# Kernel tuning notes

Hardware: AMD Instinct MI355X
Metric: run time of the kernel (lower is better)

The kernel has to match this reference:

```python
import jax, jax.numpy as jnp
import numpy as np

D_MODEL = 1024
NHEAD = 16
HEAD_DIM = D_MODEL // NHEAD


def setup_inputs() -> dict:
    key = jax.random.key(0)
    ks = jax.random.split(key, 9)
    s = 0.02
    x = jax.random.normal(ks[0], (2, 2048, D_MODEL), dtype=jnp.float32)
    Wq = jax.random.normal(ks[1], (D_MODEL, D_MODEL), dtype=jnp.float32) * s
    bq = jnp.zeros((D_MODEL,), jnp.float32)
    Wk = jax.random.normal(ks[2], (D_MODEL, D_MODEL), dtype=jnp.float32) * s
    bk = jnp.zeros((D_MODEL,), jnp.float32)
    Wv = jax.random.normal(ks[3], (D_MODEL, D_MODEL), dtype=jnp.float32) * s
    bv = jnp.zeros((D_MODEL,), jnp.float32)
    Wo = jax.random.normal(ks[4], (D_MODEL, D_MODEL), dtype=jnp.float32) * s
    bo = jnp.zeros((D_MODEL,), jnp.float32)
    return {"x": x, "Wq": Wq, "bq": bq, "Wk": Wk, "bk": bk,
            "Wv": Wv, "bv": bv, "Wo": Wo, "bo": bo}


def _rope(x, sin, cos):
    # x: [B, L, H, Dh]; rotate-half as in the torch module
    half = x.shape[-1] // 2
    x1, x2 = x[..., :half], x[..., half:]
    rotated = jnp.concatenate([-x2, x1], axis=-1)
    return x * cos + rotated * sin


def reference(x, Wq, bq, Wk, bk, Wv, bv, Wo, bo):
    B, L, D = x.shape
    H, Dh = NHEAD, HEAD_DIM
    q = (x @ Wq.T + bq).reshape(B, L, H, Dh)
    k = (x @ Wk.T + bk).reshape(B, L, H, Dh)
    v = (x @ Wv.T + bv).reshape(B, L, H, Dh)

    inv_freq = 1.0 / (10000.0 ** (jnp.arange(0, Dh, 2, dtype=jnp.float32) / Dh))
    t = jnp.arange(L, dtype=jnp.float32)
    freqs = jnp.einsum('i,j->ij', t, inv_freq)          # [L, Dh/2]
    emb = jnp.concatenate([freqs, freqs], axis=-1)      # [L, Dh]
    cos = jnp.cos(emb)[None, :, None, :]
    sin = jnp.sin(emb)[None, :, None, :]

    q = _rope(q, sin, cos)
    k = _rope(k, sin, cos)

    # [B, H, L, L]
    scores = jnp.einsum('bqhd,bkhd->bhqk', q, k) / jnp.sqrt(jnp.float32(Dh))
    attn = jax.nn.softmax(scores, axis=-1)
    # dropout in eval mode = identity (p given as 0.0)
    out = jnp.einsum('bhqk,bkhd->bqhd', attn, v).reshape(B, L, D)
    return out @ Wo.T + bo
```

## Files before the change

### kernel.cpp

```cpp
#include <hip/hip_runtime.h>
#include <math.h>

#define D_MODEL 1024
#define NHEAD 16
#define HEAD_DIM 64
#define L_SEQ 2048
#define BATCH 2
#define M_ROWS 4096
#define SC_Q 0.18033688011112042f

typedef __attribute__((ext_vector_type(8))) short short8;
typedef __attribute__((ext_vector_type(4))) float floatx4;

__device__ inline unsigned f2bf_u(float x) {
    unsigned u = __float_as_uint(x);
    return (u + 0x7fffu + ((u >> 16) & 1u)) >> 16;
}

__device__ inline void gl_lds16(const void* g, void* l) {
    __builtin_amdgcn_global_load_lds((const __attribute__((address_space(1))) void*)g,
                                     (__attribute__((address_space(3))) void*)l, 16, 0, 0);
}

__global__ __launch_bounds__(256) void cvt_all(
    const float* __restrict__ x,  const float* __restrict__ wq,
    const float* __restrict__ wk, const float* __restrict__ wv,
    const float* __restrict__ wo,
    unsigned short* __restrict__ xb,  unsigned short* __restrict__ wqb,
    unsigned short* __restrict__ wkb, unsigned short* __restrict__ wvb,
    unsigned short* __restrict__ wob, float* __restrict__ rt) {
    if (blockIdx.y == 5) {
        for (int idx = blockIdx.x * 256 + threadIdx.x; idx < L_SEQ * 16;
             idx += gridDim.x * 256) {
            int l = idx >> 4, f = idx & 15;
            float if0 = (float)pow(10000.0, -(double)f / 32.0);
            float if1 = (float)pow(10000.0, -(double)(f + 16) / 32.0);
            float s0, c0, s1, c1;
            sincosf((float)l * if0, &s0, &c0);
            sincosf((float)l * if1, &s1, &c1);
            float4 v = {c0, c1, s0, s1};
            *(float4*)(rt + (size_t)idx * 4) = v;
        }
        return;
    }
    const float* s; unsigned short* d; int n;
    switch (blockIdx.y) {
        case 0:  s = x;  d = xb;  n = M_ROWS * D_MODEL; break;
        case 1:  s = wq; d = wqb; n = D_MODEL * D_MODEL; break;
        case 2:  s = wk; d = wkb; n = D_MODEL * D_MODEL; break;
        case 3:  s = wv; d = wvb; n = D_MODEL * D_MODEL; break;
        default: s = wo; d = wob; n = D_MODEL * D_MODEL; break;
    }
    int stride = gridDim.x * 256 * 4;
    for (int i = (blockIdx.x * 256 + threadIdx.x) * 4; i < n; i += stride) {
        float4 v = *(const float4*)(s + i);
        ushort4 o;
        o.x = (unsigned short)f2bf_u(v.x);
        o.y = (unsigned short)f2bf_u(v.y);
        o.z = (unsigned short)f2bf_u(v.z);
        o.w = (unsigned short)f2bf_u(v.w);
        *(ushort4*)(d + i) = o;
    }
}

__global__ __launch_bounds__(256) void gemm_qkv(
    const unsigned short* __restrict__ xb,
    const unsigned short* __restrict__ wqb, const unsigned short* __restrict__ wkb,
    const unsigned short* __restrict__ wvb,
    const float* __restrict__ bq, const float* __restrict__ bk,
    const float* __restrict__ bv, const float* __restrict__ rt,
    unsigned short* __restrict__ qo, unsigned short* __restrict__ ko,
    unsigned short* __restrict__ vo) {
    __shared__ __align__(16) unsigned short As[128 * 32];
    __shared__ __align__(16) unsigned short Bs[128 * 32];

    const int K = D_MODEL;
    const int tid = threadIdx.x;
    const int lane = tid & 63;
    const int w = tid >> 6;
    const int wm = (w & 1) * 64;
    const int wn = (w >> 1) * 64;
    const int m0 = blockIdx.x * 128;
    const int n0 = blockIdx.y * 128;

    const unsigned short* Wsel; const float* bsel;
    unsigned short* osel; int mode; float oscale;
    if (blockIdx.z == 0)      { Wsel = wqb; bsel = bq; osel = qo; mode = 1; oscale = SC_Q; }
    else if (blockIdx.z == 1) { Wsel = wkb; bsel = bk; osel = ko; mode = 1; oscale = 1.0f; }
    else                      { Wsel = wvb; bsel = bv; osel = vo; mode = 2; oscale = 1.0f; }

    floatx4 acc[4][4];
#pragma unroll
    for (int i = 0; i < 4; ++i)
#pragma unroll
        for (int j = 0; j < 4; ++j) acc[i][j] = (floatx4){0.f, 0.f, 0.f, 0.f};

    const int sr = lane >> 2;
    const int ss = lane & 3;
    const unsigned short* Ag = xb + (size_t)m0 * K;
    const unsigned short* Bg = Wsel + (size_t)n0 * K;

    for (int k0 = 0; k0 < K; k0 += 32) {
        __syncthreads();
#pragma unroll
        for (int t = 0; t < 2; ++t) {
            int R0 = t * 64 + w * 16;
            int r = R0 + sr;
            int c = ss ^ ((r >> 1) & 3);
            gl_lds16(Ag + (size_t)r * K + k0 + c * 8, (void*)(As + R0 * 32));
            gl_lds16(Bg + (size_t)r * K + k0 + c * 8, (void*)(Bs + R0 * 32));
        }
        __syncthreads();

        short8 af[4], bf[4];
#pragma unroll
        for (int mt = 0; mt < 4; ++mt) {
            int ar = wm + mt * 16 + (lane & 15);
            int slot = (lane >> 4) ^ ((ar >> 1) & 3);
            af[mt] = *(const short8*)(As + ar * 32 + slot * 8);
        }
#pragma unroll
        for (int nt = 0; nt < 4; ++nt) {
            int br = wn + nt * 16 + (lane & 15);
            int slot = (lane >> 4) ^ ((br >> 1) & 3);
            bf[nt] = *(const short8*)(Bs + br * 32 + slot * 8);
        }
#pragma unroll
        for (int mt = 0; mt < 4; ++mt)
#pragma unroll
            for (int nt = 0; nt < 4; ++nt)
                acc[mt][nt] = __builtin_amdgcn_mfma_f32_16x16x32_bf16(
                    af[mt], bf[nt], acc[mt][nt], 0, 0, 0);
    }

#pragma unroll
    for (int nt = 0; nt < 4; ++nt) {
        float bn = bsel[n0 + wn + nt * 16 + (lane & 15)];
#pragma unroll
        for (int mt = 0; mt < 4; ++mt)
#pragma unroll
            for (int i = 0; i < 4; ++i) acc[mt][nt][i] += bn;
    }

    const int h = (n0 + wn) >> 6;

    if (mode == 1) {
#pragma unroll
        for (int mt = 0; mt < 4; ++mt)
#pragma unroll
            for (int i = 0; i < 4; ++i) {
                int m = m0 + wm + mt * 16 + (lane >> 4) * 4 + i;
                int b = m >> 11, l = m & (L_SEQ - 1);
                float4 tc = *(const float4*)(rt + ((size_t)(l * 16 + (lane & 15)) << 2));
#pragma unroll
                for (int nt = 0; nt < 4; ++nt) {
                    int dh = nt * 16 + (lane & 15);
                    float partner = acc[mt][nt ^ 2][i];
                    float rot = (nt < 2) ? -partner : partner;
                    float c = (nt & 1) ? tc.y : tc.x;
                    float s = (nt & 1) ? tc.w : tc.z;
                    float val = (acc[mt][nt][i] * c + rot * s) * oscale;
                    size_t idx = (((size_t)(b * NHEAD + h)) * L_SEQ + l) * HEAD_DIM + dh;
                    osel[idx] = (unsigned short)f2bf_u(val);
                }
            }
    } else {
#pragma unroll
        for (int mt = 0; mt < 4; ++mt)
#pragma unroll
            for (int ih = 0; ih < 4; ih += 2) {
                int m = m0 + wm + mt * 16 + (lane >> 4) * 4 + ih;
                int b = m >> 11, l = m & (L_SEQ - 1);
#pragma unroll
                for (int nt = 0; nt < 4; ++nt) {
                    int dh = nt * 16 + (lane & 15);
                    unsigned v0 = f2bf_u(acc[mt][nt][ih]);
                    unsigned v1 = f2bf_u(acc[mt][nt][ih + 1]);
                    size_t idx = (((size_t)(b * NHEAD + h)) * HEAD_DIM + dh) * L_SEQ + l;
                    *(unsigned*)(vo + idx) = v0 | (v1 << 16);
                }
            }
    }
}

__global__ __launch_bounds__(256) void gemm_out(
    const unsigned short* __restrict__ A, const unsigned short* __restrict__ Wb,
    const float* __restrict__ bias, float* __restrict__ out) {
    __shared__ __align__(16) unsigned short As[128 * 32];
    __shared__ __align__(16) unsigned short Bs[128 * 32];

    const int K = D_MODEL;
    const int tid = threadIdx.x;
    const int lane = tid & 63;
    const int w = tid >> 6;
    const int wm = (w & 1) * 64;
    const int wn = (w >> 1) * 64;
    const int m0 = blockIdx.x * 128;
    const int n0 = blockIdx.y * 128;

    floatx4 acc[4][4];
#pragma unroll
    for (int i = 0; i < 4; ++i)
#pragma unroll
        for (int j = 0; j < 4; ++j) acc[i][j] = (floatx4){0.f, 0.f, 0.f, 0.f};

    const int sr = lane >> 2;
    const int ss = lane & 3;
    const unsigned short* Ag = A + (size_t)m0 * K;
    const unsigned short* Bg = Wb + (size_t)n0 * K;

    for (int k0 = 0; k0 < K; k0 += 32) {
        __syncthreads();
#pragma unroll
        for (int t = 0; t < 2; ++t) {
            int R0 = t * 64 + w * 16;
            int r = R0 + sr;
            int c = ss ^ ((r >> 1) & 3);
            gl_lds16(Ag + (size_t)r * K + k0 + c * 8, (void*)(As + R0 * 32));
            gl_lds16(Bg + (size_t)r * K + k0 + c * 8, (void*)(Bs + R0 * 32));
        }
        __syncthreads();

        short8 af[4], bf[4];
#pragma unroll
        for (int mt = 0; mt < 4; ++mt) {
            int ar = wm + mt * 16 + (lane & 15);
            int slot = (lane >> 4) ^ ((ar >> 1) & 3);
            af[mt] = *(const short8*)(As + ar * 32 + slot * 8);
        }
#pragma unroll
        for (int nt = 0; nt < 4; ++nt) {
            int br = wn + nt * 16 + (lane & 15);
            int slot = (lane >> 4) ^ ((br >> 1) & 3);
            bf[nt] = *(const short8*)(Bs + br * 32 + slot * 8);
        }
#pragma unroll
        for (int mt = 0; mt < 4; ++mt)
#pragma unroll
            for (int nt = 0; nt < 4; ++nt)
                acc[mt][nt] = __builtin_amdgcn_mfma_f32_16x16x32_bf16(
                    af[mt], bf[nt], acc[mt][nt], 0, 0, 0);
    }

#pragma unroll
    for (int nt = 0; nt < 4; ++nt) {
        int n = n0 + wn + nt * 16 + (lane & 15);
        float bn = bias[n];
#pragma unroll
        for (int mt = 0; mt < 4; ++mt)
#pragma unroll
            for (int i = 0; i < 4; ++i) {
                int m = m0 + wm + mt * 16 + (lane >> 4) * 4 + i;
                out[(size_t)m * D_MODEL + n] = acc[mt][nt][i] + bn;
            }
    }
}

__global__ __launch_bounds__(256) void attn_mfma(
    const unsigned short* __restrict__ q, const unsigned short* __restrict__ k,
    const unsigned short* __restrict__ vt, unsigned short* __restrict__ out) {
    __shared__ __align__(16) unsigned short Ks[2][64 * 64];
    __shared__ __align__(16) unsigned short Vs[2][64 * 64];
    __shared__ __align__(16) unsigned short Ps[4 * 32 * 72];

    const int tid = threadIdx.x;
    const int lane = tid & 63;
    const int w = tid >> 6;
    const int bh = blockIdx.y;
    const int q0 = blockIdx.x * 128;

    const unsigned short* qb = q + (size_t)bh * L_SEQ * HEAD_DIM;
    const unsigned short* kb = k + (size_t)bh * L_SEQ * HEAD_DIM;
    const unsigned short* vb = vt + (size_t)bh * HEAD_DIM * L_SEQ;

    short8 qf[2][2];
#pragma unroll
    for (int mt = 0; mt < 2; ++mt)
#pragma unroll
        for (int ks = 0; ks < 2; ++ks)
            qf[mt][ks] = *(const short8*)(
                qb + (size_t)(q0 + w * 32 + mt * 16 + (lane & 15)) * HEAD_DIM
                + ks * 32 + (lane >> 4) * 8);

    floatx4 o[2][4];
    float lsum[2][4];
#pragma unroll
    for (int mt = 0; mt < 2; ++mt)
#pragma unroll
        for (int j = 0; j < 4; ++j) {
            o[mt][j] = (floatx4){0.f, 0.f, 0.f, 0.f};
            lsum[mt][j & 3] = 0.f;
        }

    unsigned short* Psw = Ps + w * (32 * 72);
    const int sr = lane >> 3;
    const int ss = lane & 7;
    const int T = L_SEQ / 64;

#pragma unroll
    for (int t = 0; t < 2; ++t) {
        int R0 = t * 32 + w * 8;
        int r = R0 + sr;
        int c = ss ^ (r & 7);
        gl_lds16(kb + (size_t)r * HEAD_DIM + c * 8, (void*)(Ks[0] + R0 * 64));
        gl_lds16(vb + (size_t)r * L_SEQ + c * 8, (void*)(Vs[0] + R0 * 64));
    }

    for (int t = 0; t < T; ++t) {
        __syncthreads();
        if (t + 1 < T) {
            int kv1 = (t + 1) * 64;
            int nb = (t + 1) & 1;
#pragma unroll
            for (int tt = 0; tt < 2; ++tt) {
                int R0 = tt * 32 + w * 8;
                int r = R0 + sr;
                int c = ss ^ (r & 7);
                gl_lds16(kb + (size_t)(kv1 + r) * HEAD_DIM + c * 8, (void*)(Ks[nb] + R0 * 64));
                gl_lds16(vb + (size_t)r * L_SEQ + kv1 + c * 8, (void*)(Vs[nb] + R0 * 64));
            }
        }
        const unsigned short* Kc = Ks[t & 1];
        const unsigned short* Vc = Vs[t & 1];

        floatx4 s[2][4];
#pragma unroll
        for (int mt = 0; mt < 2; ++mt)
#pragma unroll
            for (int nt = 0; nt < 4; ++nt) s[mt][nt] = (floatx4){0.f, 0.f, 0.f, 0.f};
#pragma unroll
        for (int ks = 0; ks < 2; ++ks)
#pragma unroll
            for (int nt = 0; nt < 4; ++nt) {
                int br = nt * 16 + (lane & 15);
                int slot = (ks * 4 + (lane >> 4)) ^ (br & 7);
                short8 bfr = *(const short8*)(Kc + br * 64 + slot * 8);
                s[0][nt] = __builtin_amdgcn_mfma_f32_16x16x32_bf16(qf[0][ks], bfr, s[0][nt], 0, 0, 0);
                s[1][nt] = __builtin_amdgcn_mfma_f32_16x16x32_bf16(qf[1][ks], bfr, s[1][nt], 0, 0, 0);
            }

#pragma unroll
        for (int mt = 0; mt < 2; ++mt)
#pragma unroll
            for (int i = 0; i < 4; ++i) {
                int row = mt * 16 + (lane >> 4) * 4 + i;
#pragma unroll
                for (int nt = 0; nt < 4; ++nt) {
                    float p = exp2f(s[mt][nt][i]);
                    unsigned u = __float_as_uint(p);
                    lsum[mt][i] += __uint_as_float(u & 0xffff0000u);
                    Psw[row * 72 + nt * 16 + (lane & 15)] = (unsigned short)(u >> 16);
                }
            }

#pragma unroll
        for (int ks = 0; ks < 2; ++ks) {
            short8 a0 = *(const short8*)(Psw + (lane & 15) * 72 + (ks * 4 + (lane >> 4)) * 8);
            short8 a1 = *(const short8*)(Psw + (16 + (lane & 15)) * 72 + (ks * 4 + (lane >> 4)) * 8);
#pragma unroll
            for (int nt = 0; nt < 4; ++nt) {
                int br = nt * 16 + (lane & 15);
                int slot = (ks * 4 + (lane >> 4)) ^ (br & 7);
                short8 bfr = *(const short8*)(Vc + br * 64 + slot * 8);
                o[0][nt] = __builtin_amdgcn_mfma_f32_16x16x32_bf16(a0, bfr, o[0][nt], 0, 0, 0);
                o[1][nt] = __builtin_amdgcn_mfma_f32_16x16x32_bf16(a1, bfr, o[1][nt], 0, 0, 0);
            }
        }
    }

#pragma unroll
    for (int mt = 0; mt < 2; ++mt)
#pragma unroll
        for (int i = 0; i < 4; ++i) {
            float rs = lsum[mt][i];
            rs += __shfl_xor(rs, 1, 64);
            rs += __shfl_xor(rs, 2, 64);
            rs += __shfl_xor(rs, 4, 64);
            rs += __shfl_xor(rs, 8, 64);
            lsum[mt][i] = 1.0f / rs;
        }

    const int b = bh >> 4, h = bh & (NHEAD - 1);
#pragma unroll
    for (int mt = 0; mt < 2; ++mt)
#pragma unroll
        for (int i = 0; i < 4; ++i) {
            int l = q0 + w * 32 + mt * 16 + (lane >> 4) * 4 + i;
            float inv = lsum[mt][i];
#pragma unroll
            for (int nt = 0; nt < 4; ++nt) {
                int dh = nt * 16 + (lane & 15);
                size_t idx = ((size_t)b * L_SEQ + l) * D_MODEL + h * HEAD_DIM + dh;
                out[idx] = (unsigned short)f2bf_u(o[mt][nt][i] * inv);
            }
        }
}

extern "C" void kernel_launch(void* const* d_in, const int* in_sizes, int n_in,
                              void* d_out, int out_size, void* d_ws, size_t ws_size,
                              hipStream_t stream) {
    const float* x  = (const float*)d_in[0];
    const float* Wq = (const float*)d_in[1];
    const float* bq = (const float*)d_in[2];
    const float* Wk = (const float*)d_in[3];
    const float* bk = (const float*)d_in[4];
    const float* Wv = (const float*)d_in[5];
    const float* bv = (const float*)d_in[6];
    const float* Wo = (const float*)d_in[7];
    const float* bo = (const float*)d_in[8];
    float* outp = (float*)d_out;

    const size_t XE = (size_t)M_ROWS * D_MODEL;
    const size_t WE = (size_t)D_MODEL * D_MODEL;
    unsigned short* xb  = (unsigned short*)d_ws;
    unsigned short* wqb = xb + XE;
    unsigned short* wkb = wqb + WE;
    unsigned short* wvb = wkb + WE;
    unsigned short* wob = wvb + WE;
    unsigned short* qbf = wob + WE;
    unsigned short* kbf = qbf + XE;
    unsigned short* vtb = kbf + XE;
    unsigned short* aob = vtb + XE;
    float* rt = (float*)(aob + XE);

    cvt_all<<<dim3(1024, 6), 256, 0, stream>>>(x, Wq, Wk, Wv, Wo,
                                               xb, wqb, wkb, wvb, wob, rt);

    gemm_qkv<<<dim3(M_ROWS / 128, D_MODEL / 128, 3), 256, 0, stream>>>(
        xb, wqb, wkb, wvb, bq, bk, bv, rt, qbf, kbf, vtb);

    attn_mfma<<<dim3(L_SEQ / 128, BATCH * NHEAD), 256, 0, stream>>>(qbf, kbf, vtb, aob);

    gemm_out<<<dim3(M_ROWS / 128, D_MODEL / 128), 256, 0, stream>>>(aob, wob, bo, outp);
}
```

Before: 222.1 us.

## Split attention over KV halves with combine kernel and smaller out-GEMM tiles

Attention gains a grid z dimension that splits the KV sequence in two, doubling the number of blocks. Each half writes unnormalised fp32 partial outputs and row sums, and a new combine kernel merges them into bf16. Row sums now come from an MFMA against a ones vector instead of scalar adds. Other changes: K/V staging drops double buffering, gains a second barrier per tile and a 4-waves occupancy hint, exp2 uses the hardware builtin, and gemm_out uses 64-row tiles for more blocks. The costs are extra fp32 partial traffic, one more launch and less load/compute overlap inside the attention loop.

```diff
diff --git a/kernel.cpp b/kernel.cpp
--- a/kernel.cpp
+++ b/kernel.cpp
@@ -11,6 +11,12 @@
 
 typedef __attribute__((ext_vector_type(8))) short short8;
 typedef __attribute__((ext_vector_type(4))) float floatx4;
+
+#if __has_builtin(__builtin_amdgcn_exp2f)
+#define EXP2F(x) __builtin_amdgcn_exp2f(x)
+#else
+#define EXP2F(x) exp2f(x)
+#endif
 
 __device__ inline unsigned f2bf_u(float x) {
     unsigned u = __float_as_uint(x);
@@ -186,21 +192,21 @@
 __global__ __launch_bounds__(256) void gemm_out(
     const unsigned short* __restrict__ A, const unsigned short* __restrict__ Wb,
     const float* __restrict__ bias, float* __restrict__ out) {
-    __shared__ __align__(16) unsigned short As[128 * 32];
+    __shared__ __align__(16) unsigned short As[64 * 32];
     __shared__ __align__(16) unsigned short Bs[128 * 32];
 
     const int K = D_MODEL;
     const int tid = threadIdx.x;
     const int lane = tid & 63;
     const int w = tid >> 6;
-    const int wm = (w & 1) * 64;
+    const int wm = (w & 1) * 32;
     const int wn = (w >> 1) * 64;
-    const int m0 = blockIdx.x * 128;
+    const int m0 = blockIdx.x * 64;
     const int n0 = blockIdx.y * 128;
 
-    floatx4 acc[4][4];
-#pragma unroll
-    for (int i = 0; i < 4; ++i)
+    floatx4 acc[2][4];
+#pragma unroll
+    for (int i = 0; i < 2; ++i)
 #pragma unroll
         for (int j = 0; j < 4; ++j) acc[i][j] = (floatx4){0.f, 0.f, 0.f, 0.f};
 
@@ -211,19 +217,23 @@
 
     for (int k0 = 0; k0 < K; k0 += 32) {
         __syncthreads();
+        {
+            int r = w * 16 + sr;
+            int c = ss ^ ((r >> 1) & 3);
+            gl_lds16(Ag + (size_t)r * K + k0 + c * 8, (void*)(As + (w * 16) * 32));
+        }
 #pragma unroll
         for (int t = 0; t < 2; ++t) {
             int R0 = t * 64 + w * 16;
             int r = R0 + sr;
             int c = ss ^ ((r >> 1) & 3);
-            gl_lds16(Ag + (size_t)r * K + k0 + c * 8, (void*)(As + R0 * 32));
             gl_lds16(Bg + (size_t)r * K + k0 + c * 8, (void*)(Bs + R0 * 32));
         }
         __syncthreads();
 
-        short8 af[4], bf[4];
-#pragma unroll
-        for (int mt = 0; mt < 4; ++mt) {
+        short8 af[2], bf[4];
+#pragma unroll
+        for (int mt = 0; mt < 2; ++mt) {
             int ar = wm + mt * 16 + (lane & 15);
             int slot = (lane >> 4) ^ ((ar >> 1) & 3);
             af[mt] = *(const short8*)(As + ar * 32 + slot * 8);
@@ -235,7 +245,7 @@
             bf[nt] = *(const short8*)(Bs + br * 32 + slot * 8);
         }
 #pragma unroll
-        for (int mt = 0; mt < 4; ++mt)
+        for (int mt = 0; mt < 2; ++mt)
 #pragma unroll
             for (int nt = 0; nt < 4; ++nt)
                 acc[mt][nt] = __builtin_amdgcn_mfma_f32_16x16x32_bf16(
@@ -247,7 +257,7 @@
         int n = n0 + wn + nt * 16 + (lane & 15);
         float bn = bias[n];
 #pragma unroll
-        for (int mt = 0; mt < 4; ++mt)
+        for (int mt = 0; mt < 2; ++mt)
 #pragma unroll
             for (int i = 0; i < 4; ++i) {
                 int m = m0 + wm + mt * 16 + (lane >> 4) * 4 + i;
@@ -256,11 +266,14 @@
     }
 }
 
-__global__ __launch_bounds__(256) void attn_mfma(
+template <int NZ>
+__global__ __launch_bounds__(256, 4) void attn_mfma(
     const unsigned short* __restrict__ q, const unsigned short* __restrict__ k,
-    const unsigned short* __restrict__ vt, unsigned short* __restrict__ out) {
-    __shared__ __align__(16) unsigned short Ks[2][64 * 64];
-    __shared__ __align__(16) unsigned short Vs[2][64 * 64];
+    const unsigned short* __restrict__ vt,
+    float* __restrict__ opart, float* __restrict__ lpart,
+    unsigned short* __restrict__ ao) {
+    __shared__ __align__(16) unsigned short Ks[64 * 64];
+    __shared__ __align__(16) unsigned short Vs[64 * 64];
     __shared__ __align__(16) unsigned short Ps[4 * 32 * 72];
 
     const int tid = threadIdx.x;
@@ -268,6 +281,8 @@
     const int w = tid >> 6;
     const int bh = blockIdx.y;
     const int q0 = blockIdx.x * 128;
+    const int z = blockIdx.z;
+    const int kvbase = z * (L_SEQ / NZ);
 
     const unsigned short* qb = q + (size_t)bh * L_SEQ * HEAD_DIM;
     const unsigned short* kb = k + (size_t)bh * L_SEQ * HEAD_DIM;
@@ -283,45 +298,34 @@
                 + ks * 32 + (lane >> 4) * 8);
 
     floatx4 o[2][4];
-    float lsum[2][4];
-#pragma unroll
-    for (int mt = 0; mt < 2; ++mt)
-#pragma unroll
-        for (int j = 0; j < 4; ++j) {
-            o[mt][j] = (floatx4){0.f, 0.f, 0.f, 0.f};
-            lsum[mt][j & 3] = 0.f;
-        }
+    floatx4 ls[2];
+#pragma unroll
+    for (int mt = 0; mt < 2; ++mt) {
+        ls[mt] = (floatx4){0.f, 0.f, 0.f, 0.f};
+#pragma unroll
+        for (int j = 0; j < 4; ++j) o[mt][j] = (floatx4){0.f, 0.f, 0.f, 0.f};
+    }
+
+    short8 ones;
+#pragma unroll
+    for (int j = 0; j < 8; ++j) ones[j] = (short)0x3F80;
 
     unsigned short* Psw = Ps + w * (32 * 72);
     const int sr = lane >> 3;
     const int ss = lane & 7;
-    const int T = L_SEQ / 64;
-
-#pragma unroll
-    for (int t = 0; t < 2; ++t) {
-        int R0 = t * 32 + w * 8;
-        int r = R0 + sr;
-        int c = ss ^ (r & 7);
-        gl_lds16(kb + (size_t)r * HEAD_DIM + c * 8, (void*)(Ks[0] + R0 * 64));
-        gl_lds16(vb + (size_t)r * L_SEQ + c * 8, (void*)(Vs[0] + R0 * 64));
-    }
-
-    for (int t = 0; t < T; ++t) {
-        __syncthreads();
-        if (t + 1 < T) {
-            int kv1 = (t + 1) * 64;
-            int nb = (t + 1) & 1;
-#pragma unroll
-            for (int tt = 0; tt < 2; ++tt) {
-                int R0 = tt * 32 + w * 8;
-                int r = R0 + sr;
-                int c = ss ^ (r & 7);
-                gl_lds16(kb + (size_t)(kv1 + r) * HEAD_DIM + c * 8, (void*)(Ks[nb] + R0 * 64));
-                gl_lds16(vb + (size_t)r * L_SEQ + kv1 + c * 8, (void*)(Vs[nb] + R0 * 64));
-            }
-        }
-        const unsigned short* Kc = Ks[t & 1];
-        const unsigned short* Vc = Vs[t & 1];
+
+    for (int t = 0; t < L_SEQ / (64 * NZ); ++t) {
+        int kv0 = kvbase + t * 64;
+        __syncthreads();
+#pragma unroll
+        for (int tt = 0; tt < 2; ++tt) {
+            int R0 = tt * 32 + w * 8;
+            int r = R0 + sr;
+            int c = ss ^ (r & 7);
+            gl_lds16(kb + (size_t)(kv0 + r) * HEAD_DIM + c * 8, (void*)(Ks + R0 * 64));
+            gl_lds16(vb + (size_t)r * L_SEQ + kv0 + c * 8, (void*)(Vs + R0 * 64));
+        }
+        __syncthreads();
 
         floatx4 s[2][4];
 #pragma unroll
@@ -334,7 +338,7 @@
             for (int nt = 0; nt < 4; ++nt) {
                 int br = nt * 16 + (lane & 15);
                 int slot = (ks * 4 + (lane >> 4)) ^ (br & 7);
-                short8 bfr = *(const short8*)(Kc + br * 64 + slot * 8);
+                short8 bfr = *(const short8*)(Ks + br * 64 + slot * 8);
                 s[0][nt] = __builtin_amdgcn_mfma_f32_16x16x32_bf16(qf[0][ks], bfr, s[0][nt], 0, 0, 0);
                 s[1][nt] = __builtin_amdgcn_mfma_f32_16x16x32_bf16(qf[1][ks], bfr, s[1][nt], 0, 0, 0);
             }
@@ -346,10 +350,9 @@
                 int row = mt * 16 + (lane >> 4) * 4 + i;
 #pragma unroll
                 for (int nt = 0; nt < 4; ++nt) {
-                    float p = exp2f(s[mt][nt][i]);
-                    unsigned u = __float_as_uint(p);
-                    lsum[mt][i] += __uint_as_float(u & 0xffff0000u);
-                    Psw[row * 72 + nt * 16 + (lane & 15)] = (unsigned short)(u >> 16);
+                    float p = EXP2F(s[mt][nt][i]);
+                    Psw[row * 72 + nt * 16 + (lane & 15)] =
+                        (unsigned short)(__float_as_uint(p) >> 16);
                 }
             }
 
@@ -357,43 +360,77 @@
         for (int ks = 0; ks < 2; ++ks) {
             short8 a0 = *(const short8*)(Psw + (lane & 15) * 72 + (ks * 4 + (lane >> 4)) * 8);
             short8 a1 = *(const short8*)(Psw + (16 + (lane & 15)) * 72 + (ks * 4 + (lane >> 4)) * 8);
+            ls[0] = __builtin_amdgcn_mfma_f32_16x16x32_bf16(a0, ones, ls[0], 0, 0, 0);
+            ls[1] = __builtin_amdgcn_mfma_f32_16x16x32_bf16(a1, ones, ls[1], 0, 0, 0);
 #pragma unroll
             for (int nt = 0; nt < 4; ++nt) {
                 int br = nt * 16 + (lane & 15);
                 int slot = (ks * 4 + (lane >> 4)) ^ (br & 7);
-                short8 bfr = *(const short8*)(Vc + br * 64 + slot * 8);
+                short8 bfr = *(const short8*)(Vs + br * 64 + slot * 8);
                 o[0][nt] = __builtin_amdgcn_mfma_f32_16x16x32_bf16(a0, bfr, o[0][nt], 0, 0, 0);
                 o[1][nt] = __builtin_amdgcn_mfma_f32_16x16x32_bf16(a1, bfr, o[1][nt], 0, 0, 0);
             }
         }
     }
 
-#pragma unroll
-    for (int mt = 0; mt < 2; ++mt)
-#pragma unroll
-        for (int i = 0; i < 4; ++i) {
-            float rs = lsum[mt][i];
-            rs += __shfl_xor(rs, 1, 64);
-            rs += __shfl_xor(rs, 2, 64);
-            rs += __shfl_xor(rs, 4, 64);
-            rs += __shfl_xor(rs, 8, 64);
-            lsum[mt][i] = 1.0f / rs;
-        }
-
-    const int b = bh >> 4, h = bh & (NHEAD - 1);
-#pragma unroll
-    for (int mt = 0; mt < 2; ++mt)
-#pragma unroll
-        for (int i = 0; i < 4; ++i) {
-            int l = q0 + w * 32 + mt * 16 + (lane >> 4) * 4 + i;
-            float inv = lsum[mt][i];
-#pragma unroll
-            for (int nt = 0; nt < 4; ++nt) {
-                int dh = nt * 16 + (lane & 15);
-                size_t idx = ((size_t)b * L_SEQ + l) * D_MODEL + h * HEAD_DIM + dh;
-                out[idx] = (unsigned short)f2bf_u(o[mt][nt][i] * inv);
-            }
-        }
+    if (NZ == 1) {
+        const int b = bh >> 4, h = bh & (NHEAD - 1);
+#pragma unroll
+        for (int mt = 0; mt < 2; ++mt)
+#pragma unroll
+            for (int i = 0; i < 4; ++i) {
+                int l = q0 + w * 32 + mt * 16 + (lane >> 4) * 4 + i;
+                float inv = 1.0f / ls[mt][i];
+#pragma unroll
+                for (int nt = 0; nt < 4; ++nt) {
+                    int dh = nt * 16 + (lane & 15);
+                    size_t idx = ((size_t)b * L_SEQ + l) * D_MODEL + h * HEAD_DIM + dh;
+                    ao[idx] = (unsigned short)f2bf_u(o[mt][nt][i] * inv);
+                }
+            }
+    } else {
+        const size_t base = ((size_t)z * (BATCH * NHEAD) + bh) * L_SEQ;
+#pragma unroll
+        for (int mt = 0; mt < 2; ++mt)
+#pragma unroll
+            for (int i = 0; i < 4; ++i) {
+                int l = q0 + w * 32 + mt * 16 + (lane >> 4) * 4 + i;
+#pragma unroll
+                for (int nt = 0; nt < 4; ++nt) {
+                    int dh = nt * 16 + (lane & 15);
+                    opart[(base + l) * HEAD_DIM + dh] = o[mt][nt][i];
+                }
+            }
+        if ((lane & 15) == 0) {
+#pragma unroll
+            for (int mt = 0; mt < 2; ++mt)
+#pragma unroll
+                for (int i = 0; i < 4; ++i) {
+                    int l = q0 + w * 32 + mt * 16 + (lane >> 4) * 4 + i;
+                    lpart[base + l] = ls[mt][i];
+                }
+        }
+    }
+}
+
+__global__ __launch_bounds__(256) void attn_combine(
+    const float* __restrict__ opart, const float* __restrict__ lpart,
+    unsigned short* __restrict__ ao) {
+    const size_t R = (size_t)BATCH * NHEAD * L_SEQ;
+    int e = blockIdx.x * 256 + threadIdx.x;
+    int r = e >> 4;
+    int dh0 = (e & 15) * 4;
+    float4 a = *(const float4*)(opart + (size_t)r * HEAD_DIM + dh0);
+    float4 c = *(const float4*)(opart + (R + r) * HEAD_DIM + dh0);
+    float inv = 1.0f / (lpart[r] + lpart[R + r]);
+    int bh = r >> 11, l = r & (L_SEQ - 1);
+    int b = bh >> 4, h = bh & (NHEAD - 1);
+    ushort4 ov;
+    ov.x = (unsigned short)f2bf_u((a.x + c.x) * inv);
+    ov.y = (unsigned short)f2bf_u((a.y + c.y) * inv);
+    ov.z = (unsigned short)f2bf_u((a.z + c.z) * inv);
+    ov.w = (unsigned short)f2bf_u((a.w + c.w) * inv);
+    *(ushort4*)(ao + ((size_t)b * L_SEQ + l) * D_MODEL + h * HEAD_DIM + dh0) = ov;
 }
 
 extern "C" void kernel_launch(void* const* d_in, const int* in_sizes, int n_in,
@@ -412,16 +449,22 @@
 
     const size_t XE = (size_t)M_ROWS * D_MODEL;
     const size_t WE = (size_t)D_MODEL * D_MODEL;
-    unsigned short* xb  = (unsigned short*)d_ws;
-    unsigned short* wqb = xb + XE;
+    unsigned short* wqb = (unsigned short*)d_ws;
     unsigned short* wkb = wqb + WE;
     unsigned short* wvb = wkb + WE;
     unsigned short* wob = wvb + WE;
     unsigned short* qbf = wob + WE;
     unsigned short* kbf = qbf + XE;
     unsigned short* vtb = kbf + XE;
-    unsigned short* aob = vtb + XE;
-    float* rt = (float*)(aob + XE);
+    unsigned short* xb  = vtb + XE;
+    unsigned short* aob = xb;
+    float* rt    = (float*)(xb + XE);
+    float* lpart = rt;
+    float* opart = rt + 131072;
+
+    const size_t base_bytes  = (4 * WE + 4 * XE) * 2 + 131072 * 4;
+    const size_t split_bytes = base_bytes + (size_t)8 * 1024 * 1024 * 4;
+    const bool use_split = ws_size >= split_bytes;
 
     cvt_all<<<dim3(1024, 6), 256, 0, stream>>>(x, Wq, Wk, Wv, Wo,
                                                xb, wqb, wkb, wvb, wob, rt);
@@ -429,7 +472,14 @@
     gemm_qkv<<<dim3(M_ROWS / 128, D_MODEL / 128, 3), 256, 0, stream>>>(
         xb, wqb, wkb, wvb, bq, bk, bv, rt, qbf, kbf, vtb);
 
-    attn_mfma<<<dim3(L_SEQ / 128, BATCH * NHEAD), 256, 0, stream>>>(qbf, kbf, vtb, aob);
-
-    gemm_out<<<dim3(M_ROWS / 128, D_MODEL / 128), 256, 0, stream>>>(aob, wob, bo, outp);
-}
+    if (use_split) {
+        attn_mfma<2><<<dim3(L_SEQ / 128, BATCH * NHEAD, 2), 256, 0, stream>>>(
+            qbf, kbf, vtb, opart, lpart, nullptr);
+        attn_combine<<<dim3(4096), 256, 0, stream>>>(opart, lpart, aob);
+    } else {
+        attn_mfma<1><<<dim3(L_SEQ / 128, BATCH * NHEAD, 1), 256, 0, stream>>>(
+            qbf, kbf, vtb, nullptr, nullptr, aob);
+    }
+
+    gemm_out<<<dim3(M_ROWS / 64, D_MODEL / 128), 256, 0, stream>>>(aob, wob, bo, outp);
+}
```

Result: faster. 196.3 us (-11.6%).
